# Kernel optimization log

Hardware: AMD Instinct MI355X
Metric: run time of the kernel (lower is better)

## Reference

```python
import jax, jax.numpy as jnp
import numpy as np

B, T, D, H = 1, 2049, 1024, 16
HD = D // H                      # head_dim = 64
MAX_SEQ = 1025
L = 2 * MAX_SEQ - 1              # = T (required by the module's relative shift)

def setup_inputs() -> dict:
    key = jax.random.key(0)
    ks = jax.random.split(key, 12)
    s = 0.02
    return {
        'q': jax.random.normal(ks[0], (B, T, D), dtype=jnp.float32),
        'k': jax.random.normal(ks[1], (B, T, D), dtype=jnp.float32),
        'v': jax.random.normal(ks[2], (B, T, D), dtype=jnp.float32),
        'mask': jnp.tril(jnp.ones((1, 1, T, T), dtype=jnp.int32)),  # causal
        'Wq_w': jax.random.normal(ks[3], (D, D), dtype=jnp.float32) * s,
        'Wq_b': jnp.zeros((D,), dtype=jnp.float32),
        'Wk_w': jax.random.normal(ks[4], (D, D), dtype=jnp.float32) * s,
        'Wk_b': jnp.zeros((D,), dtype=jnp.float32),
        'Wv_w': jax.random.normal(ks[5], (D, D), dtype=jnp.float32) * s,
        'Wv_b': jnp.zeros((D,), dtype=jnp.float32),
        'Er': jax.random.normal(ks[6], (L, HD), dtype=jnp.float32),
        'Wo_w': jax.random.normal(ks[7], (D, D), dtype=jnp.float32) * s,
        'Wo_b': jnp.zeros((D,), dtype=jnp.float32),
    }

def reference(q, k, v, mask, Wq_w, Wq_b, Wk_w, Wk_b, Wv_w, Wv_b, Er, Wo_w, Wo_b):
    b, t, d = q.shape
    def proj(x, w, bias):
        # nn.Linear: x @ W^T + b ; then (B,T,H,HD) -> (B,H,T,HD)
        return (x @ w.T + bias).reshape(b, t, H, HD).transpose(0, 2, 1, 3)
    qh = proj(q, Wq_w, Wq_b)
    kh = proj(k, Wk_w, Wk_b)
    vh = proj(v, Wv_w, Wv_b)
    scores = jnp.einsum('bhtd,bhsd->bhts', qh, kh)          # (B,H,T,T)
    QEr = jnp.einsum('bhtd,ld->bhtl', qh, Er)               # (B,H,T,L) with L == T
    # _relative_shift: pad a zero row on seq dim then drop first row ->
    # row i becomes QEr row i+1, last row zeros (faithful to torch code)
    rel = jnp.concatenate([QEr[:, :, 1:, :], jnp.zeros_like(QEr[:, :, :1, :])], axis=2)
    scores = scores + rel
    scores = jnp.where(mask[:, :, :t, :t] == 0, -jnp.inf, scores)
    attn = jax.nn.softmax(scores / (HD ** 0.5), axis=-1)
    ctx = jnp.einsum('bhts,bhsd->bthd', attn, vh).reshape(b, t, d)
    return ctx @ Wo_w.T + Wo_b
```

## Files before the change

### kernel.cpp

```cpp
#include <hip/hip_runtime.h>
#include <hip/hip_bf16.h>
#include <math.h>

constexpr int T_SEQ = 2049;
constexpr int D_MODEL = 1024;
constexpr int N_HEAD = 16;
constexpr int HEAD_DIM = 64;
constexpr int VT_STRIDE = 2112;
constexpr int T1_ROWS = 1152;

typedef __attribute__((ext_vector_type(8))) short short8;
typedef __attribute__((ext_vector_type(4))) short short4v;
typedef __attribute__((ext_vector_type(4))) float floatx4;

__device__ inline void load_lds16(const void* g, void* l) {
  __builtin_amdgcn_global_load_lds(
      (const __attribute__((address_space(1))) unsigned int*)g,
      (__attribute__((address_space(3))) unsigned int*)l, 16, 0, 0);
}

__device__ inline short8 cvt8_bf16(const float* p) {
  float4 a = *(const float4*)p, b = *(const float4*)(p + 4);
  __hip_bfloat16 t[8] = {__float2bfloat16(a.x), __float2bfloat16(a.y),
                         __float2bfloat16(a.z), __float2bfloat16(a.w),
                         __float2bfloat16(b.x), __float2bfloat16(b.y),
                         __float2bfloat16(b.z), __float2bfloat16(b.w)};
  return *(const short8*)t;
}

__device__ inline float bf2f(__hip_bfloat16 x) { return __bfloat162float(x); }

__global__ __launch_bounds__(256) void cast_all(
    const float* __restrict__ q, const float* __restrict__ k,
    const float* __restrict__ v, const float* __restrict__ wq,
    const float* __restrict__ wk, const float* __restrict__ wv,
    const float* __restrict__ er, const float* __restrict__ wo,
    __hip_bfloat16* __restrict__ qo, __hip_bfloat16* __restrict__ ko,
    __hip_bfloat16* __restrict__ vo, __hip_bfloat16* __restrict__ wqo,
    __hip_bfloat16* __restrict__ wko, __hip_bfloat16* __restrict__ wvo,
    __hip_bfloat16* __restrict__ ero, __hip_bfloat16* __restrict__ woo) {
  const int z = blockIdx.y;
  const float* in;
  __hip_bfloat16* out;
  int n;
  switch (z) {
    case 0: in = q; out = qo; n = T_SEQ * D_MODEL; break;
    case 1: in = k; out = ko; n = T_SEQ * D_MODEL; break;
    case 2: in = v; out = vo; n = T_SEQ * D_MODEL; break;
    case 3: in = wq; out = wqo; n = D_MODEL * D_MODEL; break;
    case 4: in = wk; out = wko; n = D_MODEL * D_MODEL; break;
    case 5: in = wv; out = wvo; n = D_MODEL * D_MODEL; break;
    case 6: in = er; out = ero; n = T_SEQ * HEAD_DIM; break;
    default: in = wo; out = woo; n = D_MODEL * D_MODEL; break;
  }
  const int i = (blockIdx.x * 256 + threadIdx.x) * 8;
  if (i + 8 > n) return;
  *(short8*)(out + i) = cvt8_bf16(in + i);
}

template <int BN, int OUTK>
__global__ __launch_bounds__(256) void mfma_gemm(
    const __hip_bfloat16* __restrict__ A0, const __hip_bfloat16* __restrict__ A1,
    const __hip_bfloat16* __restrict__ A2, const __hip_bfloat16* __restrict__ W0,
    const __hip_bfloat16* __restrict__ W1, const __hip_bfloat16* __restrict__ W2,
    const float* __restrict__ bias0, const float* __restrict__ bias1,
    const float* __restrict__ bias2, void* C0, void* C1, void* C2, int M) {
  constexpr int K = D_MODEL;
  constexpr int BK = 32;
  constexpr int NSTAGE = K / BK;
  constexpr int NT = BN / 32;
  constexpr int AINST = 2;
  constexpr int BINST = BN / 64;
  constexpr int NLOADS = AINST + BINST;
  constexpr int ABYTES = 128 * BK * 2;
  constexpr int BBYTES = BN * BK * 2;
  __shared__ __align__(16) char smem[3 * (ABYTES + BBYTES)];
  __hip_bfloat16* As = (__hip_bfloat16*)smem;
  __hip_bfloat16* Bs = (__hip_bfloat16*)(smem + 3 * ABYTES);

  const int z = blockIdx.z;
  const short* A = (const short*)(z == 0 ? A0 : z == 1 ? A1 : A2);
  const short* W = (const short*)(z == 0 ? W0 : z == 1 ? W1 : W2);
  const float* bias = z == 0 ? bias0 : z == 1 ? bias1 : bias2;
  void* C = z == 0 ? C0 : z == 1 ? C1 : C2;

  const int tid = threadIdx.x;
  const int wave = tid >> 6, lane = tid & 63;
  const int col = lane & 15, quad = lane >> 4;
  const int wm = wave >> 1, wn = wave & 1;
  const int m0 = blockIdx.y * 128, n0 = blockIdx.x * BN;

  const int srow = lane >> 2;
  const int sslot = lane & 3;

  floatx4 acc[4][NT];
#pragma unroll
  for (int i = 0; i < 4; i++)
#pragma unroll
    for (int j = 0; j < NT; j++) acc[i][j] = (floatx4){0.f, 0.f, 0.f, 0.f};

#define STAGE_G(K0, BUF)                                                      \
  {                                                                           \
    _Pragma("unroll") for (int i = 0; i < AINST; i++) {                       \
      const int r_ = (wave * AINST + i) * 16 + srow;                          \
      const int ch = sslot ^ ((r_ >> 1) & 3);                                 \
      const int am = min(m0 + r_, M - 1);                                     \
      load_lds16(A + (size_t)am * K + (K0) + ch * 8,                          \
                 (char*)As + (BUF)*ABYTES + (wave * AINST + i) * 1024);       \
    }                                                                         \
    _Pragma("unroll") for (int i = 0; i < BINST; i++) {                       \
      const int r_ = (wave * BINST + i) * 16 + srow;                          \
      const int ch = sslot ^ ((r_ >> 1) & 3);                                 \
      load_lds16(W + (size_t)(n0 + r_) * K + (K0) + ch * 8,                   \
                 (char*)Bs + (BUF)*BBYTES + (wave * BINST + i) * 1024);       \
    }                                                                         \
  }

  STAGE_G(0, 0)
  STAGE_G(BK, 1)

  for (int s = 0; s < NSTAGE; ++s) {
    const int buf = s % 3;
    if (s + 2 < NSTAGE) {
      STAGE_G((s + 2) * BK, (s + 2) % 3)
      asm volatile("s_waitcnt vmcnt(%0)" ::"i"(2 * NLOADS) : "memory");
    } else if (s + 1 < NSTAGE) {
      asm volatile("s_waitcnt vmcnt(%0)" ::"i"(NLOADS) : "memory");
    } else {
      asm volatile("s_waitcnt vmcnt(0)" ::: "memory");
    }
    __builtin_amdgcn_s_barrier();

    const __hip_bfloat16* as = As + buf * (ABYTES / 2);
    const __hip_bfloat16* bs = Bs + buf * (BBYTES / 2);
    short8 af[4], bfr[NT];
#pragma unroll
    for (int t = 0; t < 4; t++) {
      const int ra = wm * 64 + t * 16 + col;
      af[t] = *(const short8*)(as + ra * 32 + ((quad ^ ((ra >> 1) & 3)) * 8));
    }
#pragma unroll
    for (int t = 0; t < NT; t++) {
      const int rb = wn * (BN / 2) + t * 16 + col;
      bfr[t] = *(const short8*)(bs + rb * 32 + ((quad ^ ((rb >> 1) & 3)) * 8));
    }
#pragma unroll
    for (int mt = 0; mt < 4; mt++)
#pragma unroll
      for (int nt = 0; nt < NT; nt++)
        acc[mt][nt] = __builtin_amdgcn_mfma_f32_16x16x32_bf16(af[mt], bfr[nt],
                                                              acc[mt][nt], 0, 0, 0);
    asm volatile("" ::: "memory");
    __builtin_amdgcn_s_barrier();
  }
#undef STAGE_G

  if (OUTK == 2 && z == 2) {
    short* Tt = (short*)smem;
#pragma unroll
    for (int mt = 0; mt < 4; mt++) {
      const int mb = wm * 16 + mt * 4 + quad;
#pragma unroll
      for (int nt = 0; nt < NT; nt++) {
        const int n = wn * (BN / 2) + nt * 16 + col;
        const float bb = bias[n0 + n];
        __hip_bfloat16 pk[4];
#pragma unroll
        for (int r = 0; r < 4; r++) pk[r] = __float2bfloat16(acc[mt][nt][r] + bb);
        *(short4v*)((char*)Tt + n * 256 + ((mb ^ (n & 15)) << 3)) =
            *(const short4v*)pk;
      }
    }
    __syncthreads();
    const int n_loc = tid >> 1, half = tid & 1;
    if (m0 + half * 64 < VT_STRIDE) {
      const int ng = n0 + n_loc;
      __hip_bfloat16* dst = (__hip_bfloat16*)C +
                            ((size_t)(ng >> 6) * HEAD_DIM + (ng & 63)) * VT_STRIDE +
                            m0 + half * 64;
#pragma unroll
      for (int c = 0; c < 8; c++) {
        short4v lo = *(const short4v*)((char*)Tt + n_loc * 256 +
                                       (((half * 16 + 2 * c) ^ (n_loc & 15)) << 3));
        short4v hi = *(const short4v*)((char*)Tt + n_loc * 256 +
                                       (((half * 16 + 2 * c + 1) ^ (n_loc & 15)) << 3));
        short8 o8 = {lo[0], lo[1], lo[2], lo[3], hi[0], hi[1], hi[2], hi[3]};
        *(short8*)((short*)dst + c * 8) = o8;
      }
    }
    return;
  }

#pragma unroll
  for (int mt = 0; mt < 4; mt++) {
#pragma unroll
    for (int r = 0; r < 4; r++) {
      const int m = m0 + wm * 64 + mt * 16 + quad * 4 + r;
      if (m >= M) continue;
#pragma unroll
      for (int nt = 0; nt < NT; nt++) {
        const int n = n0 + wn * (BN / 2) + nt * 16 + col;
        const float val = acc[mt][nt][r] + bias[n];
        if (OUTK == 0) {
          ((float*)C)[(size_t)m * D_MODEL + n] = val;
        } else {
          const int h = n >> 6, hd = n & 63;
          ((__hip_bfloat16*)C)[((size_t)h * T_SEQ + m) * HEAD_DIM + hd] =
              __float2bfloat16(val);
        }
      }
    }
  }
}

__global__ __launch_bounds__(512, 4) void flash_attn(
    const __hip_bfloat16* __restrict__ qh, const __hip_bfloat16* __restrict__ kh,
    const __hip_bfloat16* __restrict__ er, const __hip_bfloat16* __restrict__ vt,
    __hip_bfloat16* __restrict__ ctx, __hip_bfloat16* __restrict__ O0,
    __hip_bfloat16* __restrict__ O1, float* __restrict__ l0g,
    float* __restrict__ l1g) {
  __shared__ __align__(16) __hip_bfloat16 Ks[2][64 * 128];
  __shared__ __align__(16) __hip_bfloat16 Vs[2][64 * 64];
  __shared__ __align__(16) __hip_bfloat16 Ps[8][1024];

  const int tid = threadIdx.x;
  const int id = blockIdx.x + 26 * blockIdx.y;
  const int slot = id >> 3;
  const int h = (id & 7) + 8 * (slot >= 26);
  const int b = 25 - (slot >= 26 ? slot - 26 : slot);

  const int qt = (b < 8) ? b : 8 + ((b - 8) >> 1);
  const int tq0 = qt * 128;
  const int jmax = min(tq0 + 127, T_SEQ - 1) >> 6;
  int j0, j1;
  bool alt;
  if (b < 8) {
    j0 = 0; j1 = jmax; alt = false;
  } else {
    const int mid = (jmax + 1) >> 1;
    alt = (b - 8) & 1;
    j0 = alt ? mid : 0;
    j1 = alt ? jmax : mid - 1;
  }

  const int wave = tid >> 6;
  const int lane = tid & 63;
  const int col = lane & 15;
  const int quad = lane >> 4;

  const short* qplane = (const short*)(qh + (size_t)h * T_SEQ * HEAD_DIM);
  const short* kplane = (const short*)(kh + (size_t)h * T_SEQ * HEAD_DIM);
  const short* eplane = (const short*)er;
  const short* vplane = (const short*)(vt + (size_t)h * HEAD_DIM * VT_STRIDE);

  const int t_abs = tq0 + wave * 16 + col;
  const int tload = min(t_abs, T_SEQ - 1);
  const bool hiz = (t_abs >= T_SEQ - 1);
  short8 aq[4];
#pragma unroll
  for (int kc = 0; kc < 4; kc++) {
    short8 v = *(const short8*)(qplane + (size_t)tload * 64 + kc * 32 + quad * 8);
    if (kc >= 2 && hiz) v = (short8){0, 0, 0, 0, 0, 0, 0, 0};
    aq[kc] = v;
  }

  floatx4 o[4];
  float l_lane = 0.f;
#pragma unroll
  for (int i = 0; i < 4; i++) o[i] = (floatx4){0.f, 0.f, 0.f, 0.f};

  const int tstrip = tq0 + wave * 16;
  __hip_bfloat16* psw = &Ps[wave][0];

#define STAGE_TILE(JJ, BUF)                                                        \
  {                                                                                \
    const int s0_ = (JJ) * 64;                                                     \
    _Pragma("unroll") for (int ii = 0; ii < 2; ii++) {                             \
      const int i_ = wave * 2 + ii;                                                \
      const int r_ = i_ * 4 + (lane >> 4);                                         \
      const int sl_ = lane & 15;                                                   \
      const int g_ = (sl_ & 8) | ((sl_ ^ (r_ & 7)) & 7);                           \
      const int s_ = min(s0_ + r_, T_SEQ - 1);                                     \
      const short* src_ = (g_ < 8) ? (kplane + (size_t)s_ * 64 + g_ * 8)           \
                                   : (eplane + (size_t)s_ * 64 + (g_ - 8) * 8);    \
      load_lds16(src_, (char*)&Ks[BUF][0] + i_ * 1024);                            \
    }                                                                              \
    {                                                                              \
      const int d_ = wave * 8 + (lane >> 3);                                       \
      const int sl_ = lane & 7;                                                    \
      const int g_ = sl_ ^ (d_ & 7);                                               \
      load_lds16(vplane + (size_t)d_ * VT_STRIDE + s0_ + g_ * 8,                   \
                 (char*)&Vs[BUF][0] + wave * 1024);                                \
    }                                                                              \
  }

  STAGE_TILE(j0, 0)
  int buf = 0;

  for (int j = j0; j <= j1; ++j, buf ^= 1) {
    __syncthreads();
    if (j < j1) STAGE_TILE(j + 1, buf ^ 1)

    const int s0 = j * 64;
    if (s0 > tstrip + 15) continue;

    const __hip_bfloat16* ks = &Ks[buf][0];
    const __hip_bfloat16* vs = &Vs[buf][0];

    floatx4 sacc[4];
    __builtin_amdgcn_s_setprio(1);
#pragma unroll
    for (int st = 0; st < 4; st++) {
      floatx4 c = {0.f, 0.f, 0.f, 0.f};
      const int row = st * 16 + col;
#pragma unroll
      for (int kc = 0; kc < 4; kc++) {
        const int ch = kc * 4 + quad;
        const int slot2 = (ch & 8) | ((ch ^ (row & 7)) & 7);
        short8 ka = *(const short8*)(ks + row * 128 + slot2 * 8);
        c = __builtin_amdgcn_mfma_f32_16x16x32_bf16(ka, aq[kc], c, 0, 0, 0);
      }
      sacc[st] = c;
    }
    __builtin_amdgcn_s_setprio(0);

    if (s0 + 63 > tstrip) {
#pragma unroll
      for (int st = 0; st < 4; st++) {
        const int sbase = s0 + st * 16 + quad * 4;
#pragma unroll
        for (int r = 0; r < 4; r++)
          if (sbase + r > t_abs) sacc[st][r] = -INFINITY;
      }
    }

    float rs = 0.f;
#pragma unroll
    for (int st = 0; st < 4; st++)
#pragma unroll
      for (int r = 0; r < 4; r++) {
        const float p = __expf(sacc[st][r] * 0.125f);
        sacc[st][r] = p;
        rs += p;
      }
    l_lane += rs;

#pragma unroll
    for (int st = 0; st < 4; st++) {
      __hip_bfloat16 pb[4];
#pragma unroll
      for (int r = 0; r < 4; r++) pb[r] = __float2bfloat16(sacc[st][r]);
      const int kcA = st >> 1;
      const int quadA = (st & 1) * 2 + (quad >> 1);
      const int off = ((kcA * 4 + quadA) * 16 + col) * 8 + (quad & 1) * 4;
      *(short4v*)(psw + off) = *(const short4v*)pb;
    }
    short8 pa[2];
#pragma unroll
    for (int kc = 0; kc < 2; kc++)
      pa[kc] = *(const short8*)(psw + ((kc * 4 + quad) * 16 + col) * 8);

    __builtin_amdgcn_s_setprio(1);
#pragma unroll
    for (int nt = 0; nt < 4; nt++) {
      const int row = nt * 16 + col;
#pragma unroll
      for (int kc = 0; kc < 2; kc++) {
        const int slot2 = (kc * 4 + quad) ^ (row & 7);
        short8 vb = *(const short8*)(vs + row * 64 + slot2 * 8);
        o[nt] = __builtin_amdgcn_mfma_f32_16x16x32_bf16(pa[kc], vb, o[nt], 0, 0, 0);
      }
    }
    __builtin_amdgcn_s_setprio(0);
  }

  l_lane += __shfl_xor(l_lane, 16, 64);
  l_lane += __shfl_xor(l_lane, 32, 64);

  if (b < 8) {
    const float linv = 1.0f / l_lane;
    float linv_r[4];
#pragma unroll
    for (int r = 0; r < 4; r++) linv_r[r] = __shfl(linv, quad * 4 + r, 64);
#pragma unroll
    for (int r = 0; r < 4; r++) {
      const int t = tstrip + quad * 4 + r;
#pragma unroll
      for (int nt = 0; nt < 4; nt++)
        ctx[(size_t)t * D_MODEL + h * 64 + nt * 16 + col] =
            __float2bfloat16(o[nt][r] * linv_r[r]);
    }
  } else {
    if (lane < 16) {
      const int t = tstrip + lane;
      if (t < T_SEQ) {
        if (!alt)
          l0g[h * T1_ROWS + (t - 1024)] = l_lane;
        else
          l1g[h * T1_ROWS + (t - 1024)] = l_lane;
      }
    }
#pragma unroll
    for (int r = 0; r < 4; r++) {
      const int t = tstrip + quad * 4 + r;
      if (t < T_SEQ) {
        __hip_bfloat16* dst = (!alt ? O0 : O1) + (size_t)(t - 1024) * D_MODEL;
#pragma unroll
        for (int nt = 0; nt < 4; nt++)
          dst[h * 64 + nt * 16 + col] = __float2bfloat16(o[nt][r]);
      }
    }
  }
}

__global__ __launch_bounds__(256) void finalize(
    const __hip_bfloat16* __restrict__ O0, const __hip_bfloat16* __restrict__ O1,
    const float* __restrict__ l0g, const float* __restrict__ l1g,
    __hip_bfloat16* __restrict__ ctx) {
  const int idx = blockIdx.x * 256 + threadIdx.x;
  const int tr = idx >> 7;
  const int t = 1024 + tr;
  if (t >= T_SEQ) return;
  const int ch = idx & 127;
  const int h = ch >> 3;

  const float l = l0g[h * T1_ROWS + tr] + l1g[h * T1_ROWS + tr];
  const __hip_bfloat16* a = O0 + (size_t)tr * D_MODEL + ch * 8;
  const __hip_bfloat16* bsrc = O1 + (size_t)tr * D_MODEL + ch * 8;
  const float inv = 1.0f / l;
  __hip_bfloat16 outv[8];
#pragma unroll
  for (int i = 0; i < 8; i++)
    outv[i] = __float2bfloat16((bf2f(a[i]) + bf2f(bsrc[i])) * inv);
  *(short8*)(ctx + (size_t)t * D_MODEL + ch * 8) = *(const short8*)outv;
}

extern "C" void kernel_launch(void* const* d_in, const int* in_sizes, int n_in,
                              void* d_out, int out_size, void* d_ws, size_t ws_size,
                              hipStream_t stream) {
  const float* q = (const float*)d_in[0];
  const float* k = (const float*)d_in[1];
  const float* v = (const float*)d_in[2];
  const float* Wq_w = (const float*)d_in[4];
  const float* Wq_b = (const float*)d_in[5];
  const float* Wk_w = (const float*)d_in[6];
  const float* Wk_b = (const float*)d_in[7];
  const float* Wv_w = (const float*)d_in[8];
  const float* Wv_b = (const float*)d_in[9];
  const float* Er = (const float*)d_in[10];
  const float* Wo_w = (const float*)d_in[11];
  const float* Wo_b = (const float*)d_in[12];
  float* out = (float*)d_out;

  char* ws = (char*)d_ws;
  const size_t sz_plane = (size_t)T_SEQ * D_MODEL * 2;
  const size_t sz_w = (size_t)D_MODEL * D_MODEL * 2;
  const size_t sz_vt = (size_t)N_HEAD * HEAD_DIM * VT_STRIDE * 2;
  const size_t sz_er = (size_t)T_SEQ * HEAD_DIM * 2;
  const size_t sz_Op = (size_t)T1_ROWS * D_MODEL * 2;
  const size_t sz_l = (size_t)N_HEAD * T1_ROWS * 4;

  __hip_bfloat16* qbf = (__hip_bfloat16*)ws;
  __hip_bfloat16* kbf = (__hip_bfloat16*)(ws + sz_plane);
  __hip_bfloat16* vbf = (__hip_bfloat16*)(ws + 2 * sz_plane);
  __hip_bfloat16* wqb = (__hip_bfloat16*)(ws + 3 * sz_plane);
  __hip_bfloat16* wkb = (__hip_bfloat16*)(ws + 3 * sz_plane + sz_w);
  __hip_bfloat16* wvb = (__hip_bfloat16*)(ws + 3 * sz_plane + 2 * sz_w);
  char* hi = ws + 3 * sz_plane + 3 * sz_w;
  __hip_bfloat16* qpr = (__hip_bfloat16*)hi;
  __hip_bfloat16* kpr = (__hip_bfloat16*)(hi + sz_plane);
  __hip_bfloat16* vt = (__hip_bfloat16*)(hi + 2 * sz_plane);
  __hip_bfloat16* er_bf = (__hip_bfloat16*)(hi + 2 * sz_plane + sz_vt);
  __hip_bfloat16* wob = (__hip_bfloat16*)(hi + 2 * sz_plane + sz_vt + sz_er);

  __hip_bfloat16* ctxb = (__hip_bfloat16*)ws;
  __hip_bfloat16* O0 = (__hip_bfloat16*)(ws + sz_plane);
  __hip_bfloat16* O1 = (__hip_bfloat16*)(ws + sz_plane + sz_Op);
  float* l0g = (float*)(ws + sz_plane + 2 * sz_Op);
  float* l1g = (float*)(ws + sz_plane + 2 * sz_Op + sz_l);

  const dim3 blk(256);

  cast_all<<<dim3(1025, 8), blk, 0, stream>>>(q, k, v, Wq_w, Wk_w, Wv_w, Er, Wo_w,
                                              qbf, kbf, vbf, wqb, wkb, wvb, er_bf,
                                              wob);

  mfma_gemm<128, 2><<<dim3(8, 17, 3), blk, 0, stream>>>(
      qbf, kbf, vbf, wqb, wkb, wvb, Wq_b, Wk_b, Wv_b, qpr, kpr, vt, T_SEQ);

  flash_attn<<<dim3(26, N_HEAD), dim3(512), 0, stream>>>(qpr, kpr, er_bf, vt, ctxb,
                                                         O0, O1, l0g, l1g);

  finalize<<<dim3((1025 * 128 + 255) / 256), blk, 0, stream>>>(O0, O1, l0g, l1g,
                                                               ctxb);

  mfma_gemm<64, 0><<<dim3(16, 17, 1), blk, 0, stream>>>(
      ctxb, ctxb, ctxb, wob, wob, wob, Wo_b, Wo_b, Wo_b, out, out, out, T_SEQ);
}
```

Baseline: 193.6 us.

## Replace templated GEMM with specialized QKV and output GEMMs using grouped tile ordering

Splits the generic GEMM into a 512-thread QKV projection kernel and a 64x64-tile output-projection kernel. Both use a 1D grid remapped so neighbouring blocks share weight and activation tiles in L2, and double buffering replaces triple buffering. The Er bf16 cast is folded into spare blocks of the QKV kernel. The cast kernel still also writes er_bf, so the work is duplicated. Smaller output tiles raise the block count and occupancy but lower the reuse per block.

Result: faster. 180.8 us (-6.6%).

```diff
diff --git a/kernel.cpp b/kernel.cpp
--- a/kernel.cpp
+++ b/kernel.cpp
@@ -58,156 +58,242 @@
   *(short8*)(out + i) = cvt8_bf16(in + i);
 }
 
-template <int BN, int OUTK>
-__global__ __launch_bounds__(256) void mfma_gemm(
-    const __hip_bfloat16* __restrict__ A0, const __hip_bfloat16* __restrict__ A1,
-    const __hip_bfloat16* __restrict__ A2, const __hip_bfloat16* __restrict__ W0,
-    const __hip_bfloat16* __restrict__ W1, const __hip_bfloat16* __restrict__ W2,
-    const float* __restrict__ bias0, const float* __restrict__ bias1,
-    const float* __restrict__ bias2, void* C0, void* C1, void* C2, int M) {
-  constexpr int K = D_MODEL;
-  constexpr int BK = 32;
-  constexpr int NSTAGE = K / BK;
-  constexpr int NT = BN / 32;
-  constexpr int AINST = 2;
-  constexpr int BINST = BN / 64;
-  constexpr int NLOADS = AINST + BINST;
-  constexpr int ABYTES = 128 * BK * 2;
-  constexpr int BBYTES = BN * BK * 2;
-  __shared__ __align__(16) char smem[3 * (ABYTES + BBYTES)];
-  __hip_bfloat16* As = (__hip_bfloat16*)smem;
-  __hip_bfloat16* Bs = (__hip_bfloat16*)(smem + 3 * ABYTES);
-
-  const int z = blockIdx.z;
-  const short* A = (const short*)(z == 0 ? A0 : z == 1 ? A1 : A2);
-  const short* W = (const short*)(z == 0 ? W0 : z == 1 ? W1 : W2);
-  const float* bias = z == 0 ? bias0 : z == 1 ? bias1 : bias2;
-  void* C = z == 0 ? C0 : z == 1 ? C1 : C2;
+__global__ __launch_bounds__(512) void qkv_gemm8(
+    const __hip_bfloat16* __restrict__ qbf, const __hip_bfloat16* __restrict__ kbf,
+    const __hip_bfloat16* __restrict__ vbf, const __hip_bfloat16* __restrict__ wqb,
+    const __hip_bfloat16* __restrict__ wkb, const __hip_bfloat16* __restrict__ wvb,
+    const float* __restrict__ bq, const float* __restrict__ bk,
+    const float* __restrict__ bv, __hip_bfloat16* __restrict__ qpr,
+    __hip_bfloat16* __restrict__ kpr, __hip_bfloat16* __restrict__ vt,
+    const float* __restrict__ er, __hip_bfloat16* __restrict__ er_bf) {
+  const int d = blockIdx.x;
+  const int tid = threadIdx.x;
+  if (d >= 408) {
+    const int i = ((d - 408) * 512 + tid) * 8;
+    if (i + 8 <= T_SEQ * HEAD_DIM) *(short8*)(er_bf + i) = cvt8_bf16(er + i);
+    return;
+  }
+  int x, p;
+  if (d < 384) {
+    const int g = d >> 6, rem = d & 63;
+    x = rem >> 3;
+    p = g * 8 + (rem & 7);
+  } else {
+    const int t = d - 384;
+    p = 48 + (t >> 3);
+    x = t & 7;
+  }
+  const int y = p % 17, z = p / 17;
+
+  constexpr int K = D_MODEL, BK = 32, NS = K / BK;
+  __shared__ __align__(16) char smem[32768];
+
+  const short* A = (const short*)(z == 0 ? qbf : z == 1 ? kbf : vbf);
+  const short* W = (const short*)(z == 0 ? wqb : z == 1 ? wkb : wvb);
+  const float* bias = z == 0 ? bq : z == 1 ? bk : bv;
+
+  const int wave = tid >> 6, lane = tid & 63;
+  const int col = lane & 15, quad = lane >> 4;
+  const int wm = wave >> 2, wn = wave & 3;
+  const int m0 = y * 128, n0 = x * 128;
+
+  const int srow = wave * 16 + (lane >> 2);
+  const int sch = (lane & 3) ^ ((srow >> 1) & 3);
+  const int am = min(m0 + srow, T_SEQ - 1);
+
+#define STG(K0, BUF)                                                        \
+  {                                                                         \
+    load_lds16(A + (size_t)am * K + (K0) + sch * 8,                         \
+               smem + (BUF)*8192 + wave * 1024);                            \
+    load_lds16(W + (size_t)(n0 + srow) * K + (K0) + sch * 8,                \
+               smem + 16384 + (BUF)*8192 + wave * 1024);                    \
+  }
+
+  floatx4 acc[4][2];
+#pragma unroll
+  for (int i = 0; i < 4; i++)
+#pragma unroll
+    for (int j = 0; j < 2; j++) acc[i][j] = (floatx4){0.f, 0.f, 0.f, 0.f};
+
+  STG(0, 0)
+  int buf = 0;
+  for (int k0 = 0; k0 < K; k0 += BK, buf ^= 1) {
+    if (k0 + BK < K) {
+      STG(k0 + BK, buf ^ 1)
+      asm volatile("s_waitcnt vmcnt(2)" ::: "memory");
+    } else {
+      asm volatile("s_waitcnt vmcnt(0)" ::: "memory");
+    }
+    __builtin_amdgcn_s_barrier();
+
+    const __hip_bfloat16* as = (const __hip_bfloat16*)(smem + buf * 8192);
+    const __hip_bfloat16* bs = (const __hip_bfloat16*)(smem + 16384 + buf * 8192);
+    short8 af[4], bfr[2];
+#pragma unroll
+    for (int t = 0; t < 4; t++) {
+      const int ra = wm * 64 + t * 16 + col;
+      af[t] = *(const short8*)(as + ra * 32 + ((quad ^ ((ra >> 1) & 3)) * 8));
+    }
+#pragma unroll
+    for (int t = 0; t < 2; t++) {
+      const int rb = wn * 32 + t * 16 + col;
+      bfr[t] = *(const short8*)(bs + rb * 32 + ((quad ^ ((rb >> 1) & 3)) * 8));
+    }
+#pragma unroll
+    for (int mt = 0; mt < 4; mt++)
+#pragma unroll
+      for (int nt = 0; nt < 2; nt++)
+        acc[mt][nt] = __builtin_amdgcn_mfma_f32_16x16x32_bf16(af[mt], bfr[nt],
+                                                              acc[mt][nt], 0, 0, 0);
+    asm volatile("" ::: "memory");
+    __builtin_amdgcn_s_barrier();
+  }
+#undef STG
+
+  if (z == 2) {
+    short* Tt = (short*)smem;
+#pragma unroll
+    for (int mt = 0; mt < 4; mt++) {
+      const int mb = wm * 16 + mt * 4 + quad;
+#pragma unroll
+      for (int nt = 0; nt < 2; nt++) {
+        const int n = wn * 32 + nt * 16 + col;
+        const float bb = bias[n0 + n];
+        __hip_bfloat16 pk[4];
+#pragma unroll
+        for (int r = 0; r < 4; r++) pk[r] = __float2bfloat16(acc[mt][nt][r] + bb);
+        *(short4v*)((char*)Tt + n * 256 + ((mb ^ (n & 15)) << 3)) =
+            *(const short4v*)pk;
+      }
+    }
+    __syncthreads();
+    if (tid < 256) {
+      const int n_loc = tid >> 1, half = tid & 1;
+      if (m0 + half * 64 < VT_STRIDE) {
+        const int ng = n0 + n_loc;
+        __hip_bfloat16* dst = vt +
+                              ((size_t)(ng >> 6) * HEAD_DIM + (ng & 63)) * VT_STRIDE +
+                              m0 + half * 64;
+#pragma unroll
+        for (int c = 0; c < 8; c++) {
+          short4v lo = *(const short4v*)((char*)Tt + n_loc * 256 +
+                                         (((half * 16 + 2 * c) ^ (n_loc & 15)) << 3));
+          short4v hi = *(const short4v*)((char*)Tt + n_loc * 256 +
+                                         (((half * 16 + 2 * c + 1) ^ (n_loc & 15)) << 3));
+          short8 o8 = {lo[0], lo[1], lo[2], lo[3], hi[0], hi[1], hi[2], hi[3]};
+          *(short8*)((short*)dst + c * 8) = o8;
+        }
+      }
+    }
+    return;
+  }
+
+  __hip_bfloat16* C = z == 0 ? qpr : kpr;
+#pragma unroll
+  for (int mt = 0; mt < 4; mt++) {
+#pragma unroll
+    for (int r = 0; r < 4; r++) {
+      const int m = m0 + wm * 64 + mt * 16 + quad * 4 + r;
+      if (m >= T_SEQ) continue;
+#pragma unroll
+      for (int nt = 0; nt < 2; nt++) {
+        const int n = n0 + wn * 32 + nt * 16 + col;
+        const float val = acc[mt][nt][r] + bias[n];
+        const int h = n >> 6, hd = n & 63;
+        C[((size_t)h * T_SEQ + m) * HEAD_DIM + hd] = __float2bfloat16(val);
+      }
+    }
+  }
+}
+
+__global__ __launch_bounds__(256) void out_gemm(
+    const __hip_bfloat16* __restrict__ ctxb, const __hip_bfloat16* __restrict__ wob,
+    const float* __restrict__ bias, float* __restrict__ out) {
+  const int d = blockIdx.x;
+  int x, p;
+  if (d < 512) {
+    const int g = d >> 7, rem = d & 127;
+    x = rem >> 3;
+    p = g * 8 + (rem & 7);
+  } else {
+    p = 32;
+    x = d - 512;
+  }
+  const int m0 = p * 64, n0 = x * 64;
+
+  constexpr int K = D_MODEL, BK = 32;
+  __shared__ __align__(16) char smem[16384];
 
   const int tid = threadIdx.x;
   const int wave = tid >> 6, lane = tid & 63;
   const int col = lane & 15, quad = lane >> 4;
   const int wm = wave >> 1, wn = wave & 1;
-  const int m0 = blockIdx.y * 128, n0 = blockIdx.x * BN;
-
-  const int srow = lane >> 2;
-  const int sslot = lane & 3;
-
-  floatx4 acc[4][NT];
-#pragma unroll
-  for (int i = 0; i < 4; i++)
-#pragma unroll
-    for (int j = 0; j < NT; j++) acc[i][j] = (floatx4){0.f, 0.f, 0.f, 0.f};
-
-#define STAGE_G(K0, BUF)                                                      \
-  {                                                                           \
-    _Pragma("unroll") for (int i = 0; i < AINST; i++) {                       \
-      const int r_ = (wave * AINST + i) * 16 + srow;                          \
-      const int ch = sslot ^ ((r_ >> 1) & 3);                                 \
-      const int am = min(m0 + r_, M - 1);                                     \
-      load_lds16(A + (size_t)am * K + (K0) + ch * 8,                          \
-                 (char*)As + (BUF)*ABYTES + (wave * AINST + i) * 1024);       \
-    }                                                                         \
-    _Pragma("unroll") for (int i = 0; i < BINST; i++) {                       \
-      const int r_ = (wave * BINST + i) * 16 + srow;                          \
-      const int ch = sslot ^ ((r_ >> 1) & 3);                                 \
-      load_lds16(W + (size_t)(n0 + r_) * K + (K0) + ch * 8,                   \
-                 (char*)Bs + (BUF)*BBYTES + (wave * BINST + i) * 1024);       \
-    }                                                                         \
-  }
-
-  STAGE_G(0, 0)
-  STAGE_G(BK, 1)
-
-  for (int s = 0; s < NSTAGE; ++s) {
-    const int buf = s % 3;
-    if (s + 2 < NSTAGE) {
-      STAGE_G((s + 2) * BK, (s + 2) % 3)
-      asm volatile("s_waitcnt vmcnt(%0)" ::"i"(2 * NLOADS) : "memory");
-    } else if (s + 1 < NSTAGE) {
-      asm volatile("s_waitcnt vmcnt(%0)" ::"i"(NLOADS) : "memory");
+
+  const int srow = wave * 16 + (lane >> 2);
+  const int sch = (lane & 3) ^ ((srow >> 1) & 3);
+  const int am = min(m0 + srow, T_SEQ - 1);
+  const short* A = (const short*)ctxb;
+  const short* W = (const short*)wob;
+
+#define STG(K0, BUF)                                                        \
+  {                                                                         \
+    load_lds16(A + (size_t)am * K + (K0) + sch * 8,                         \
+               smem + (BUF)*4096 + wave * 1024);                            \
+    load_lds16(W + (size_t)(n0 + srow) * K + (K0) + sch * 8,                \
+               smem + 8192 + (BUF)*4096 + wave * 1024);                     \
+  }
+
+  floatx4 acc[2][2];
+#pragma unroll
+  for (int i = 0; i < 2; i++)
+#pragma unroll
+    for (int j = 0; j < 2; j++) acc[i][j] = (floatx4){0.f, 0.f, 0.f, 0.f};
+
+  STG(0, 0)
+  int buf = 0;
+  for (int k0 = 0; k0 < K; k0 += BK, buf ^= 1) {
+    if (k0 + BK < K) {
+      STG(k0 + BK, buf ^ 1)
+      asm volatile("s_waitcnt vmcnt(2)" ::: "memory");
     } else {
       asm volatile("s_waitcnt vmcnt(0)" ::: "memory");
     }
     __builtin_amdgcn_s_barrier();
 
-    const __hip_bfloat16* as = As + buf * (ABYTES / 2);
-    const __hip_bfloat16* bs = Bs + buf * (BBYTES / 2);
-    short8 af[4], bfr[NT];
-#pragma unroll
-    for (int t = 0; t < 4; t++) {
-      const int ra = wm * 64 + t * 16 + col;
+    const __hip_bfloat16* as = (const __hip_bfloat16*)(smem + buf * 4096);
+    const __hip_bfloat16* bs = (const __hip_bfloat16*)(smem + 8192 + buf * 4096);
+    short8 af[2], bfr[2];
+#pragma unroll
+    for (int t = 0; t < 2; t++) {
+      const int ra = wm * 32 + t * 16 + col;
       af[t] = *(const short8*)(as + ra * 32 + ((quad ^ ((ra >> 1) & 3)) * 8));
     }
 #pragma unroll
-    for (int t = 0; t < NT; t++) {
-      const int rb = wn * (BN / 2) + t * 16 + col;
+    for (int t = 0; t < 2; t++) {
+      const int rb = wn * 32 + t * 16 + col;
       bfr[t] = *(const short8*)(bs + rb * 32 + ((quad ^ ((rb >> 1) & 3)) * 8));
     }
 #pragma unroll
-    for (int mt = 0; mt < 4; mt++)
-#pragma unroll
-      for (int nt = 0; nt < NT; nt++)
+    for (int mt = 0; mt < 2; mt++)
+#pragma unroll
+      for (int nt = 0; nt < 2; nt++)
         acc[mt][nt] = __builtin_amdgcn_mfma_f32_16x16x32_bf16(af[mt], bfr[nt],
                                                               acc[mt][nt], 0, 0, 0);
     asm volatile("" ::: "memory");
     __builtin_amdgcn_s_barrier();
   }
-#undef STAGE_G
-
-  if (OUTK == 2 && z == 2) {
-    short* Tt = (short*)smem;
-#pragma unroll
-    for (int mt = 0; mt < 4; mt++) {
-      const int mb = wm * 16 + mt * 4 + quad;
-#pragma unroll
-      for (int nt = 0; nt < NT; nt++) {
-        const int n = wn * (BN / 2) + nt * 16 + col;
-        const float bb = bias[n0 + n];
-        __hip_bfloat16 pk[4];
-#pragma unroll
-        for (int r = 0; r < 4; r++) pk[r] = __float2bfloat16(acc[mt][nt][r] + bb);
-        *(short4v*)((char*)Tt + n * 256 + ((mb ^ (n & 15)) << 3)) =
-            *(const short4v*)pk;
-      }
-    }
-    __syncthreads();
-    const int n_loc = tid >> 1, half = tid & 1;
-    if (m0 + half * 64 < VT_STRIDE) {
-      const int ng = n0 + n_loc;
-      __hip_bfloat16* dst = (__hip_bfloat16*)C +
-                            ((size_t)(ng >> 6) * HEAD_DIM + (ng & 63)) * VT_STRIDE +
-                            m0 + half * 64;
-#pragma unroll
-      for (int c = 0; c < 8; c++) {
-        short4v lo = *(const short4v*)((char*)Tt + n_loc * 256 +
-                                       (((half * 16 + 2 * c) ^ (n_loc & 15)) << 3));
-        short4v hi = *(const short4v*)((char*)Tt + n_loc * 256 +
-                                       (((half * 16 + 2 * c + 1) ^ (n_loc & 15)) << 3));
-        short8 o8 = {lo[0], lo[1], lo[2], lo[3], hi[0], hi[1], hi[2], hi[3]};
-        *(short8*)((short*)dst + c * 8) = o8;
-      }
-    }
-    return;
-  }
-
-#pragma unroll
-  for (int mt = 0; mt < 4; mt++) {
+#undef STG
+
+#pragma unroll
+  for (int mt = 0; mt < 2; mt++) {
 #pragma unroll
     for (int r = 0; r < 4; r++) {
-      const int m = m0 + wm * 64 + mt * 16 + quad * 4 + r;
-      if (m >= M) continue;
-#pragma unroll
-      for (int nt = 0; nt < NT; nt++) {
-        const int n = n0 + wn * (BN / 2) + nt * 16 + col;
-        const float val = acc[mt][nt][r] + bias[n];
-        if (OUTK == 0) {
-          ((float*)C)[(size_t)m * D_MODEL + n] = val;
-        } else {
-          const int h = n >> 6, hd = n & 63;
-          ((__hip_bfloat16*)C)[((size_t)h * T_SEQ + m) * HEAD_DIM + hd] =
-              __float2bfloat16(val);
-        }
+      const int m = m0 + wm * 32 + mt * 16 + quad * 4 + r;
+      if (m >= T_SEQ) continue;
+#pragma unroll
+      for (int nt = 0; nt < 2; nt++) {
+        const int n = n0 + wn * 32 + nt * 16 + col;
+        out[(size_t)m * D_MODEL + n] = acc[mt][nt][r] + bias[n];
       }
     }
   }
@@ -339,9 +425,9 @@
     for (int st = 0; st < 4; st++)
 #pragma unroll
       for (int r = 0; r < 4; r++) {
-        const float p = __expf(sacc[st][r] * 0.125f);
-        sacc[st][r] = p;
-        rs += p;
+        const float pql = __expf(sacc[st][r] * 0.125f);
+        sacc[st][r] = pql;
+        rs += pql;
       }
     l_lane += rs;
 
@@ -485,8 +571,8 @@
                                               qbf, kbf, vbf, wqb, wkb, wvb, er_bf,
                                               wob);
 
-  mfma_gemm<128, 2><<<dim3(8, 17, 3), blk, 0, stream>>>(
-      qbf, kbf, vbf, wqb, wkb, wvb, Wq_b, Wk_b, Wv_b, qpr, kpr, vt, T_SEQ);
+  qkv_gemm8<<<dim3(441), dim3(512), 0, stream>>>(
+      qbf, kbf, vbf, wqb, wkb, wvb, Wq_b, Wk_b, Wv_b, qpr, kpr, vt, Er, er_bf);
 
   flash_attn<<<dim3(26, N_HEAD), dim3(512), 0, stream>>>(qpr, kpr, er_bf, vt, ctxb,
                                                          O0, O1, l0g, l1g);
@@ -494,6 +580,5 @@
   finalize<<<dim3((1025 * 128 + 255) / 256), blk, 0, stream>>>(O0, O1, l0g, l1g,
                                                                ctxb);
 
-  mfma_gemm<64, 0><<<dim3(16, 17, 1), blk, 0, stream>>>(
-      ctxb, ctxb, ctxb, wob, wob, wob, Wo_b, Wo_b, Wo_b, out, out, out, T_SEQ);
-}
+  out_gemm<<<dim3(528), blk, 0, stream>>>(ctxb, wob, Wo_b, out);
+}
```
